# Kernel optimization log

Hardware: AMD Instinct MI355X
Metric: run time of the kernel (lower is better)

The kernel has to match this reference:

```python
import jax, jax.numpy as jnp
import numpy as np


def setup_inputs() -> dict:
    key = jax.random.key(0)
    ks = jax.random.split(key, 5)
    B, S, E, H = 2, 2048, 1024, 16
    scale = 1.0 / np.sqrt(E)
    return {
        "input": jax.random.normal(ks[0], (B, S, E), dtype=jnp.float32),
        "Wqkv": jax.random.normal(ks[1], (3 * E, E), dtype=jnp.float32) * scale,
        "bqkv": jax.random.normal(ks[2], (3 * E,), dtype=jnp.float32) * 0.01,
        "Wo": jax.random.normal(ks[3], (E, E), dtype=jnp.float32) * scale,
        "bo": jax.random.normal(ks[4], (E,), dtype=jnp.float32) * 0.01,
    }


def reference(input, Wqkv, bqkv, Wo, bo):
    H = 16
    B, S, E = input.shape
    dh = E // H
    # fused QKV projection: [B, S, 3E]
    qkv = input @ Wqkv.T + bqkv
    qkv = qkv.reshape(B, S, 3, H, dh)
    qkv = jnp.transpose(qkv, (2, 0, 3, 1, 4))  # [3, B, H, S, dh]
    q, k, v = qkv[0], qkv[1], qkv[2]
    # scores [B, H, Sq, Sk]
    scores = jnp.einsum("bhqd,bhkd->bhqk", q, k) / jnp.sqrt(jnp.float32(dh))
    # NOTE: original code softmaxes over dim=2 (the QUERY axis) — reproduced faithfully
    attn = jax.nn.softmax(scores, axis=2)
    out = jnp.einsum("bhqk,bhkd->bhqd", attn, v)  # [B, H, S, dh]
    out = jnp.transpose(out, (0, 2, 1, 3)).reshape(B, S, E)
    return out @ Wo.T + bo
```

## Files before the change

kernel.cpp:

```cpp
#include <hip/hip_runtime.h>
#include <math.h>

#define B_ 2
#define S_ 2048
#define E_ 1024
#define H_ 16
#define DH_ 64
#define NE3_ 3072
#define MTOT_ (B_*S_)
#define QSCALE_ 0.18033688011112042f

typedef __bf16 bf16;
typedef bf16 bf16x8 __attribute__((ext_vector_type(8)));
typedef bf16 bf16x4 __attribute__((ext_vector_type(4)));
typedef float f32x4 __attribute__((ext_vector_type(4)));

#define MFMA16(a,b,c) __builtin_amdgcn_mfma_f32_16x16x32_bf16(a,b,c,0,0,0)

#define F_(r) ((((r) & 7) ^ (((r) >> 3) & 7)))

__device__ inline void* lds_swz(void* base, int row, int bytecol) {
    return (char*)base + row * 128 + (bytecol ^ (F_(row) << 4));
}

__device__ inline unsigned cvt_pk_bf16(float lo, float hi) {
    unsigned r;
    asm("v_cvt_pk_bf16_f32 %0, %1, %2" : "=v"(r) : "v"(lo), "v"(hi));
    return r;
}

__device__ inline float exp2_hw(float x) {
    float r;
    asm("v_exp_f32 %0, %1" : "=v"(r) : "v"(x));
    return r;
}

__device__ inline void gload_lds16(const void* g, void* l) {
    __builtin_amdgcn_global_load_lds(
        (const __attribute__((address_space(1))) void*)g,
        (__attribute__((address_space(3))) void*)l, 16, 0, 0);
}

#define NX_ (MTOT_*E_)
#define NW_ (NE3_*E_)
#define NWO_ (E_*E_)
__global__ void k_f2b3(const float* __restrict__ x, const float* __restrict__ wq,
                       const float* __restrict__ wo,
                       bf16* __restrict__ xb, bf16* __restrict__ wqb,
                       bf16* __restrict__ wob) {
    const int i = blockIdx.x * 256 + threadIdx.x;
    const int idx = i * 4;
    const float* src; bf16* dst; int off;
    if (idx < NX_)            { src = x;  dst = xb;  off = idx; }
    else if (idx < NX_ + NW_) { src = wq; dst = wqb; off = idx - NX_; }
    else                      { src = wo; dst = wob; off = idx - NX_ - NW_; }
    float4 f = *reinterpret_cast<const float4*>(src + off);
    bf16x4 o;
    o[0] = (bf16)f.x; o[1] = (bf16)f.y; o[2] = (bf16)f.z; o[3] = (bf16)f.w;
    *reinterpret_cast<bf16x4*>(dst + off) = o;
}

template<int MODE>
__global__ __launch_bounds__(256) void k_gemm(
    const bf16* __restrict__ A, const bf16* __restrict__ W,
    const float* __restrict__ bias,
    bf16* __restrict__ Qf, bf16* __restrict__ Kf, bf16* __restrict__ Vf,
    float* __restrict__ out)
{
    constexpr int NBUF = (MODE == 0) ? 1 : 2;
    __shared__ __align__(16) bf16 At[NBUF][128*64];
    __shared__ __align__(16) bf16 Bt[NBUF][128*64];
    const int tid = threadIdx.x, lane = tid & 63, w = tid >> 6;
    const int lq = lane & 15, lh = lane >> 4;
    const int wr = w >> 1, wc = w & 1;
    const int g = blockIdx.x;
    const int nxw = (MODE == 0 ? 3 : 1);
    const int xcd = g & 7, li = g >> 3;
    const int m0 = (li & 31) * 128;
    const int n0 = (xcd * nxw + (li >> 5)) * 128;

    f32x4 acc[4][4] = {};
    const int lrow = lane >> 3, lcol = (lane & 7) * 8;

    auto stage = [&](int k0, int buf) {
        for (int c4 = 0; c4 < 4; ++c4) {
            const int c = w * 4 + c4;
            const int row = c * 8 + lrow;
            const int colx = lcol ^ (F_(row) * 8);
            gload_lds16(A + (size_t)(m0 + row) * E_ + k0 + colx, &At[buf][c * 512]);
            gload_lds16(W + (size_t)(n0 + row) * E_ + k0 + colx, &Bt[buf][c * 512]);
        }
    };
    auto compute = [&](int buf) {
        for (int ks = 0; ks < 2; ++ks) {
            const int bc = ks * 64 + 16 * lh;
            bf16x8 a[4], b[4];
            for (int j = 0; j < 4; ++j)
                a[j] = *(const bf16x8*)lds_swz(&At[buf][0], wr*64 + j*16 + lq, bc);
            for (int i = 0; i < 4; ++i)
                b[i] = *(const bf16x8*)lds_swz(&Bt[buf][0], wc*64 + i*16 + lq, bc);
            for (int i = 0; i < 4; ++i)
                for (int j = 0; j < 4; ++j)
                    acc[i][j] = MFMA16(b[i], a[j], acc[i][j]);
        }
    };

    if constexpr (MODE == 0) {
        stage(0, 0);
        __syncthreads();
        for (int kt = 0; kt < E_/64; ++kt) {
            compute(0);
            if (kt + 1 < E_/64) {
                __syncthreads();
                stage((kt + 1) * 64, 0);
                __syncthreads();
            }
        }
    } else {
        stage(0, 0);
        __syncthreads();
        int cur = 0;
        for (int kt = 0; kt < E_/64; ++kt) {
            if (kt + 1 < E_/64) stage((kt + 1) * 64, cur ^ 1);
            compute(cur);
            cur ^= 1;
            if (kt + 1 < E_/64) __syncthreads();
        }
    }

    const int mW = m0 + wr*64;
    for (int i = 0; i < 4; ++i) {
        const int n4 = n0 + wc*64 + i*16 + lh * 4;
        const float4 b4 = *reinterpret_cast<const float4*>(&bias[n4]);
        const float* bp = reinterpret_cast<const float*>(&b4);
        if constexpr (MODE == 0) {
            const int t = n4 >> 10, h = (n4 >> 6) & 15, d0 = n4 & 63;
            for (int j = 0; j < 4; ++j) {
                const int m = mW + j*16 + lq;
                const int bb_i = m >> 11, s = m & 2047;
                const size_t bh32 = ((size_t)(bb_i*H_ + h)) * 32;
                const int kt = s >> 6;
                if (t == 2) {
                    const int ksV = (s >> 5) & 1, lhV = (s >> 3) & 3, eV = s & 7;
                    for (int r = 0; r < 4; ++r) {
                        const int d = d0 + r;
                        const size_t e = ((bh32 + kt)*8 + (d>>4)*2 + ksV)*512
                                       + (lhV*16 + (d & 15))*8 + eV;
                        Vf[e] = (bf16)(acc[i][j][r] + bp[r]);
                    }
                } else {
                    bf16* dst = (t == 0) ? Qf : Kf;
                    const float sc = (t == 0) ? QSCALE_ : 1.0f;
                    const int kf = (s >> 4) & 3, lqp = s & 15;
                    const size_t e = ((bh32 + kt)*8 + kf*2 + (d0>>5))*512
                                   + (((d0>>3)&3)*16 + lqp)*8 + (d0 & 7);
                    bf16x4 o;
                    for (int r = 0; r < 4; ++r)
                        o[r] = (bf16)((acc[i][j][r] + bp[r]) * sc);
                    *reinterpret_cast<bf16x4*>(dst + e) = o;
                }
            }
        } else {
            for (int j = 0; j < 4; ++j) {
                const int m = mW + j*16 + lq;
                float4 o;
                o.x = acc[i][j][0] + bp[0];
                o.y = acc[i][j][1] + bp[1];
                o.z = acc[i][j][2] + bp[2];
                o.w = acc[i][j][3] + bp[3];
                *reinterpret_cast<float4*>(out + (size_t)m * E_ + n4) = o;
            }
        }
    }
}

__global__ __launch_bounds__(256) void k_colsum(
    const bf16* __restrict__ Qf, const bf16* __restrict__ Kf,
    bf16* __restrict__ Vf)
{
    __shared__ __align__(16) char smem[49152];
    __shared__ float rlbuf[128];
    char* Kl   = smem;
    char* Qbuf = smem + 16384;
    const int tid = threadIdx.x, lane = tid & 63, w = tid >> 6;
    const int l16 = lane * 16;
    const int g = blockIdx.x, xcd = g & 7, li = g >> 3;
    const int bh = xcd * 4 + (li >> 4);
    const int k0 = (li & 15) * 128;
    const bf16* Kbase = Kf + ((size_t)bh*32 + (k0 >> 6)) * 4096;
    const bf16* Qbase = Qf + (size_t)bh*32 * 4096;

    for (int j = 0; j < 4; ++j)
        gload_lds16(Kbase + (j*256 + tid)*8, Kl + (j*256 + w*64)*16);
    auto stageQ = [&](int qt, int buf) {
        const bf16* qb = Qbase + (size_t)qt * 8192;
        for (int j = 0; j < 4; ++j)
            gload_lds16(qb + (j*256 + tid)*8, Qbuf + buf*16384 + (j*256 + w*64)*16);
    };
    stageQ(0, 0);
    __syncthreads();

    bf16x8 bk[2][2];
    for (int f = 0; f < 2; ++f)
        for (int ks = 0; ks < 2; ++ks)
            bk[f][ks] = *(const bf16x8*)(Kl + (w*4 + f*2 + ks)*1024 + l16);

    float lsum0 = 0.f, lsum1 = 0.f;
    int cur = 0;
    for (int qt = 0; qt < S_/128; ++qt) {
        if (qt + 1 < S_/128) stageQ(qt + 1, cur ^ 1);
        #pragma unroll
        for (int qi = 0; qi < 8; ++qi) {
            f32x4 s0 = {}, s1 = {};
            #pragma unroll
            for (int ks = 0; ks < 2; ++ks) {
                bf16x8 aq = *(const bf16x8*)(Qbuf + cur*16384 + (qi*2+ks)*1024 + l16);
                s0 = MFMA16(aq, bk[0][ks], s0);
                s1 = MFMA16(aq, bk[1][ks], s1);
            }
            #pragma unroll
            for (int r = 0; r < 4; ++r) {
                lsum0 += exp2_hw(s0[r]);
                lsum1 += exp2_hw(s1[r]);
            }
        }
        cur ^= 1;
        if (qt + 1 < S_/128) __syncthreads();
    }
    lsum0 += __shfl_xor(lsum0, 16); lsum0 += __shfl_xor(lsum0, 32);
    lsum1 += __shfl_xor(lsum1, 16); lsum1 += __shfl_xor(lsum1, 32);
    if (lane < 16) {
        rlbuf[w*32 + lane]      = 1.0f / lsum0;
        rlbuf[w*32 + 16 + lane] = 1.0f / lsum1;
    }
    __syncthreads();

    bf16* Vb = Vf + ((size_t)bh*32 + (k0 >> 6)) * 4096;
    for (int c = 0; c < 4; ++c) {
        const int v = c*256 + tid;
        const int kb = (v >> 9)*64 + ((v >> 6) & 1)*32 + ((v >> 4) & 3)*8;
        bf16x8* p = reinterpret_cast<bf16x8*>(Vb + v*8);
        bf16x8 x = *p, o;
        #pragma unroll
        for (int jj = 0; jj < 8; ++jj)
            o[jj] = (bf16)((float)x[jj] * rlbuf[kb + jj]);
        *p = o;
    }
}

__global__ __launch_bounds__(256) void k_attn(
    const bf16* __restrict__ Qf, const bf16* __restrict__ Kf,
    const bf16* __restrict__ Vf, bf16* __restrict__ AO)
{
    __shared__ __align__(16) char smem[49152];
    char* QP   = smem;
    char* Kbuf = smem + 16384;
    char* Vbuf = smem + 32768;
    const int tid = threadIdx.x, lane = tid & 63, w = tid >> 6;
    const int lq = lane & 15, lh = lane >> 4;
    const int l16 = lane * 16;
    const int g = blockIdx.x, xcd = g & 7, li = g >> 3;
    const int bh = xcd * 4 + (li >> 4);
    const int q0 = (li & 15) * 128;
    const bf16* Qbase = Qf + ((size_t)bh*32 + (q0 >> 6)) * 4096;
    const bf16* KVof  = (const bf16*)0;
    const bf16* Kbase = Kf + (size_t)bh*32 * 4096;
    const bf16* Vbase = Vf + (size_t)bh*32 * 4096;
    char* Plw = QP + w * 4096;
    const int pOff = (lh >> 1) * 256 + lq * 16 + (lh & 1) * 8;

    for (int j = 0; j < 4; ++j)
        gload_lds16(Qbase + (j*256 + tid)*8, QP + (j*256 + w*64)*16);
    auto stageKV = [&](int kt, int buf) {
        const bf16* kb = Kbase + (size_t)kt * 4096;
        const bf16* vb = Vbase + (size_t)kt * 4096;
        for (int j = 0; j < 2; ++j) {
            gload_lds16(kb + (j*256 + tid)*8, Kbuf + buf*8192 + (j*256 + w*64)*16);
            gload_lds16(vb + (j*256 + tid)*8, Vbuf + buf*8192 + (j*256 + w*64)*16);
        }
    };
    stageKV(0, 0);
    __syncthreads();

    bf16x8 bq[2][2];
    for (int qi = 0; qi < 2; ++qi)
        for (int ks = 0; ks < 2; ++ks)
            bq[qi][ks] = *(const bf16x8*)(QP + w*4096 + (qi*2+ks)*1024 + l16);

    f32x4 oacc[4][2] = {};
    int cur = 0;
    for (int kt = 0; kt < S_/64; ++kt) {
        if (kt + 1 < S_/64) stageKV(kt + 1, cur ^ 1);
        char* Kc = Kbuf + cur*8192;
        char* Vc = Vbuf + cur*8192;

        #pragma unroll
        for (int kf = 0; kf < 4; ++kf) {
            f32x4 sacc[2] = {};
            #pragma unroll
            for (int ks = 0; ks < 2; ++ks) {
                bf16x8 ak = *(const bf16x8*)(Kc + (kf*2+ks)*1024 + l16);
                #pragma unroll
                for (int qi = 0; qi < 2; ++qi)
                    sacc[qi] = MFMA16(ak, bq[qi][ks], sacc[qi]);
            }
            #pragma unroll
            for (int qi = 0; qi < 2; ++qi) {
                uint2 pw;
                pw.x = cvt_pk_bf16(exp2_hw(sacc[qi][0]), exp2_hw(sacc[qi][1]));
                pw.y = cvt_pk_bf16(exp2_hw(sacc[qi][2]), exp2_hw(sacc[qi][3]));
                *(uint2*)(Plw + pOff + (kf>>1)*2048 + (kf&1)*512 + qi*1024) = pw;
            }
        }

        #pragma unroll
        for (int ks = 0; ks < 2; ++ks) {
            bf16x8 av[4], bp[2];
            #pragma unroll
            for (int df = 0; df < 4; ++df)
                av[df] = *(const bf16x8*)(Vc + (df*2+ks)*1024 + l16);
            #pragma unroll
            for (int qi = 0; qi < 2; ++qi)
                bp[qi] = *(const bf16x8*)(Plw + (ks*2+qi)*1024 + l16);
            #pragma unroll
            for (int df = 0; df < 4; ++df)
                #pragma unroll
                for (int qi = 0; qi < 2; ++qi)
                    oacc[df][qi] = MFMA16(av[df], bp[qi], oacc[df][qi]);
        }
        cur ^= 1;
        if (kt + 1 < S_/64) __syncthreads();
    }

    const int b = bh >> 4, h = bh & 15;
    #pragma unroll
    for (int df = 0; df < 4; ++df)
        #pragma unroll
        for (int qi = 0; qi < 2; ++qi) {
            const int d0 = df*16 + lh * 4;
            const int q = q0 + w*32 + qi*16 + lq;
            bf16x4 o;
            for (int r = 0; r < 4; ++r) o[r] = (bf16)oacc[df][qi][r];
            *reinterpret_cast<bf16x4*>(
                AO + ((size_t)(b*S_ + q))*E_ + h*DH_ + d0) = o;
        }
}

extern "C" void kernel_launch(void* const* d_in, const int* in_sizes, int n_in,
                              void* d_out, int out_size, void* d_ws, size_t ws_size,
                              hipStream_t stream) {
    const float* input = (const float*)d_in[0];
    const float* Wqkv  = (const float*)d_in[1];
    const float* bqkv  = (const float*)d_in[2];
    const float* Wo    = (const float*)d_in[3];
    const float* bo    = (const float*)d_in[4];
    float* out = (float*)d_out;

    char* ws = (char*)d_ws;
    bf16*  Xb   = (bf16*) (ws + 0);
    bf16*  Wqb  = (bf16*) (ws + 8388608);
    bf16*  Wob  = (bf16*) (ws + 14680064);
    bf16*  Qfg  = (bf16*) (ws + 16777216);
    bf16*  Kfg  = (bf16*) (ws + 25165824);
    bf16*  Vfg  = (bf16*) (ws + 33554432);
    bf16*  AO   = (bf16*) (ws + 41943040);

    k_f2b3<<<(NX_ + NW_ + NWO_) / 1024, 256, 0, stream>>>(
        input, Wqkv, Wo, Xb, Wqb, Wob);

    k_gemm<0><<<768, 256, 0, stream>>>(Xb, Wqb, bqkv, Qfg, Kfg, Vfg, nullptr);

    k_colsum<<<512, 256, 0, stream>>>(Qfg, Kfg, Vfg);

    k_attn<<<512, 256, 0, stream>>>(Qfg, Kfg, Vfg, AO);

    k_gemm<1><<<256, 256, 0, stream>>>(AO, Wob, bo, nullptr, nullptr, nullptr, out);
}
```

Before: 158.6 us.

## Software-pipeline attention loop: overlap QK/exp of tile t with PV of tile t-1

Restructures the attention main loop so that each iteration computes QK^T and exp for the current K tile while doing the P·V multiply for the previous tile. V gets a triple buffer and P a double buffer per wave. Q is staged through the K buffer and moved into registers up front. The intent is to give the scheduler independent MFMA and transcendental work to interleave, hiding the exp and LDS latency. The cost is more LDS (72KB instead of 48KB), which may lower occupancy, plus extra prologue and epilogue code.

```diff
diff --git a/kernel.cpp b/kernel.cpp
--- a/kernel.cpp
+++ b/kernel.cpp
@@ -252,10 +252,10 @@
     const bf16* __restrict__ Qf, const bf16* __restrict__ Kf,
     const bf16* __restrict__ Vf, bf16* __restrict__ AO)
 {
-    __shared__ __align__(16) char smem[49152];
-    char* QP   = smem;
-    char* Kbuf = smem + 16384;
-    char* Vbuf = smem + 32768;
+    __shared__ __align__(16) char smem[73728];
+    char* Kbuf  = smem;
+    char* Vbuf  = smem + 16384;
+    char* Pbase = smem + 40960;
     const int tid = threadIdx.x, lane = tid & 63, w = tid >> 6;
     const int lq = lane & 15, lh = lane >> 4;
     const int l16 = lane * 16;
@@ -263,37 +263,37 @@
     const int bh = xcd * 4 + (li >> 4);
     const int q0 = (li & 15) * 128;
     const bf16* Qbase = Qf + ((size_t)bh*32 + (q0 >> 6)) * 4096;
-    const bf16* KVof  = (const bf16*)0;
     const bf16* Kbase = Kf + (size_t)bh*32 * 4096;
     const bf16* Vbase = Vf + (size_t)bh*32 * 4096;
-    char* Plw = QP + w * 4096;
     const int pOff = (lh >> 1) * 256 + lq * 16 + (lh & 1) * 8;
 
     for (int j = 0; j < 4; ++j)
-        gload_lds16(Qbase + (j*256 + tid)*8, QP + (j*256 + w*64)*16);
-    auto stageKV = [&](int kt, int buf) {
+        gload_lds16(Qbase + (j*256 + tid)*8, Kbuf + (j*256 + w*64)*16);
+    __syncthreads();
+    bf16x8 bq[2][2];
+    #pragma unroll
+    for (int qi = 0; qi < 2; ++qi)
+        #pragma unroll
+        for (int ks = 0; ks < 2; ++ks)
+            bq[qi][ks] = *(const bf16x8*)(Kbuf + w*4096 + (qi*2+ks)*1024 + l16);
+    __syncthreads();
+
+    auto stageK = [&](int kt, int slot) {
         const bf16* kb = Kbase + (size_t)kt * 4096;
+        for (int j = 0; j < 2; ++j)
+            gload_lds16(kb + (j*256 + tid)*8, Kbuf + slot*8192 + (j*256 + w*64)*16);
+    };
+    auto stageV = [&](int kt, int slot) {
         const bf16* vb = Vbase + (size_t)kt * 4096;
-        for (int j = 0; j < 2; ++j) {
-            gload_lds16(kb + (j*256 + tid)*8, Kbuf + buf*8192 + (j*256 + w*64)*16);
-            gload_lds16(vb + (j*256 + tid)*8, Vbuf + buf*8192 + (j*256 + w*64)*16);
-        }
-    };
-    stageKV(0, 0);
-    __syncthreads();
-
-    bf16x8 bq[2][2];
-    for (int qi = 0; qi < 2; ++qi)
-        for (int ks = 0; ks < 2; ++ks)
-            bq[qi][ks] = *(const bf16x8*)(QP + w*4096 + (qi*2+ks)*1024 + l16);
+        for (int j = 0; j < 2; ++j)
+            gload_lds16(vb + (j*256 + tid)*8, Vbuf + slot*8192 + (j*256 + w*64)*16);
+    };
 
     f32x4 oacc[4][2] = {};
-    int cur = 0;
-    for (int kt = 0; kt < S_/64; ++kt) {
-        if (kt + 1 < S_/64) stageKV(kt + 1, cur ^ 1);
-        char* Kc = Kbuf + cur*8192;
-        char* Vc = Vbuf + cur*8192;
-
+
+    auto QKEXP = [&](int kslot, int ppar) {
+        char* Kc = Kbuf + kslot*8192;
+        char* Pw = Pbase + w*8192 + ppar*4096;
         #pragma unroll
         for (int kf = 0; kf < 4; ++kf) {
             f32x4 sacc[2] = {};
@@ -309,10 +309,13 @@
                 uint2 pw;
                 pw.x = cvt_pk_bf16(exp2_hw(sacc[qi][0]), exp2_hw(sacc[qi][1]));
                 pw.y = cvt_pk_bf16(exp2_hw(sacc[qi][2]), exp2_hw(sacc[qi][3]));
-                *(uint2*)(Plw + pOff + (kf>>1)*2048 + (kf&1)*512 + qi*1024) = pw;
-            }
-        }
-
+                *(uint2*)(Pw + pOff + (kf>>1)*2048 + (kf&1)*512 + qi*1024) = pw;
+            }
+        }
+    };
+    auto PV = [&](int vslot, int ppar) {
+        char* Vc = Vbuf + vslot*8192;
+        char* Pw = Pbase + w*8192 + ppar*4096;
         #pragma unroll
         for (int ks = 0; ks < 2; ++ks) {
             bf16x8 av[4], bp[2];
@@ -321,16 +324,30 @@
                 av[df] = *(const bf16x8*)(Vc + (df*2+ks)*1024 + l16);
             #pragma unroll
             for (int qi = 0; qi < 2; ++qi)
-                bp[qi] = *(const bf16x8*)(Plw + (ks*2+qi)*1024 + l16);
+                bp[qi] = *(const bf16x8*)(Pw + (ks*2+qi)*1024 + l16);
             #pragma unroll
             for (int df = 0; df < 4; ++df)
                 #pragma unroll
                 for (int qi = 0; qi < 2; ++qi)
                     oacc[df][qi] = MFMA16(av[df], bp[qi], oacc[df][qi]);
         }
-        cur ^= 1;
-        if (kt + 1 < S_/64) __syncthreads();
-    }
+    };
+
+    stageK(0, 0); stageV(0, 0);
+    __syncthreads();
+    stageK(1, 1); stageV(1, 1);
+    QKEXP(0, 0);
+    __syncthreads();
+
+    int vprev = 0, vcur = 1, vnext = 2;
+    for (int t = 1; t < 32; ++t) {
+        if (t + 1 < 32) { stageK(t + 1, (t + 1) & 1); stageV(t + 1, vnext); }
+        QKEXP(t & 1, t & 1);
+        PV(vprev, (t - 1) & 1);
+        __syncthreads();
+        const int tmp = vprev; vprev = vcur; vcur = vnext; vnext = tmp;
+    }
+    PV(vprev, 1);
 
     const int b = bh >> 4, h = bh & 15;
     #pragma unroll
```

New measurement: 161.2 us. About the same (+1.6%).

## Switch attention and column-sum kernels to 32x32 MFMA with register-resident P

Applied to the files above, without the earlier changes.

Rewrites the Q/K/V fragment layouts written by the QKV GEMM epilogue to match 32x32x16 MFMA operands. The column-sum and attention kernels now use 32x32 MFMA tiles. In the attention kernel, the exp'd score fragment is repacked in registers via permlane32_swap and fed straight into the PV MFMA instead of going through LDS. It also adds s_setprio around the MFMA bursts. The aim is to remove the LDS round-trip for P and cut per-MFMA issue overhead, at the cost of a riskier layout change across three kernels.

```diff
diff --git a/kernel.cpp b/kernel.cpp
--- a/kernel.cpp
+++ b/kernel.cpp
@@ -14,8 +14,12 @@
 typedef bf16 bf16x8 __attribute__((ext_vector_type(8)));
 typedef bf16 bf16x4 __attribute__((ext_vector_type(4)));
 typedef float f32x4 __attribute__((ext_vector_type(4)));
+typedef float f32x16 __attribute__((ext_vector_type(16)));
+typedef unsigned u32x2 __attribute__((ext_vector_type(2)));
+typedef unsigned u32x4 __attribute__((ext_vector_type(4)));
 
 #define MFMA16(a,b,c) __builtin_amdgcn_mfma_f32_16x16x32_bf16(a,b,c,0,0,0)
+#define MFMA32(a,b,c) __builtin_amdgcn_mfma_f32_32x32x16_bf16(a,b,c,0,0,0)
 
 #define F_(r) ((((r) & 7) ^ (((r) >> 3) & 7)))
 
@@ -27,6 +31,11 @@
     unsigned r;
     asm("v_cvt_pk_bf16_f32 %0, %1, %2" : "=v"(r) : "v"(lo), "v"(hi));
     return r;
+}
+
+__device__ inline void permswap32(unsigned &x, unsigned &y) {
+    u32x2 r = __builtin_amdgcn_permlane32_swap(x, y, false, false);
+    x = r.x; y = r.y;
 }
 
 __device__ inline float exp2_hw(float x) {
@@ -138,22 +147,23 @@
             for (int j = 0; j < 4; ++j) {
                 const int m = mW + j*16 + lq;
                 const int bb_i = m >> 11, s = m & 2047;
-                const size_t bh32 = ((size_t)(bb_i*H_ + h)) * 32;
-                const int kt = s >> 6;
+                const size_t bhb = ((size_t)(bb_i*H_ + h)) * 131072;
                 if (t == 2) {
-                    const int ksV = (s >> 5) & 1, lhV = (s >> 3) & 3, eV = s & 7;
                     for (int r = 0; r < 4; ++r) {
                         const int d = d0 + r;
-                        const size_t e = ((bh32 + kt)*8 + (d>>4)*2 + ksV)*512
-                                       + (lhV*16 + (d & 15))*8 + eV;
+                        const size_t e = bhb + (size_t)(s >> 6) * 4096
+                                       + ((d >> 5) * 4 + ((s >> 4) & 3)) * 512
+                                       + ((d & 31) + 32 * ((s >> 3) & 1)) * 8
+                                       + (s & 7);
                         Vf[e] = (bf16)(acc[i][j][r] + bp[r]);
                     }
                 } else {
                     bf16* dst = (t == 0) ? Qf : Kf;
                     const float sc = (t == 0) ? QSCALE_ : 1.0f;
-                    const int kf = (s >> 4) & 3, lqp = s & 15;
-                    const size_t e = ((bh32 + kt)*8 + kf*2 + (d0>>5))*512
-                                   + (((d0>>3)&3)*16 + lqp)*8 + (d0 & 7);
+                    const size_t e = bhb + (size_t)(s >> 6) * 4096
+                                   + (((s >> 5) & 1) * 4 + (d0 >> 4)) * 512
+                                   + ((s & 31) + 32 * ((d0 >> 3) & 1)) * 8
+                                   + (d0 & 7);
                     bf16x4 o;
                     for (int r = 0; r < 4; ++r)
                         o[r] = (bf16)((acc[i][j][r] + bp[r]) * sc);
@@ -187,8 +197,8 @@
     const int g = blockIdx.x, xcd = g & 7, li = g >> 3;
     const int bh = xcd * 4 + (li >> 4);
     const int k0 = (li & 15) * 128;
-    const bf16* Kbase = Kf + ((size_t)bh*32 + (k0 >> 6)) * 4096;
-    const bf16* Qbase = Qf + (size_t)bh*32 * 4096;
+    const bf16* Kbase = Kf + (size_t)bh * 131072 + (size_t)(k0 >> 6) * 4096;
+    const bf16* Qbase = Qf + (size_t)bh * 131072;
 
     for (int j = 0; j < 4; ++j)
         gload_lds16(Kbase + (j*256 + tid)*8, Kl + (j*256 + w*64)*16);
@@ -200,45 +210,41 @@
     stageQ(0, 0);
     __syncthreads();
 
-    bf16x8 bk[2][2];
-    for (int f = 0; f < 2; ++f)
-        for (int ks = 0; ks < 2; ++ks)
-            bk[f][ks] = *(const bf16x8*)(Kl + (w*4 + f*2 + ks)*1024 + l16);
-
-    float lsum0 = 0.f, lsum1 = 0.f;
+    bf16x8 bk[4];
+    #pragma unroll
+    for (int sl = 0; sl < 4; ++sl)
+        bk[sl] = *(const bf16x8*)(Kl + w*4096 + sl*1024 + l16);
+
+    float lsum = 0.f;
     int cur = 0;
     for (int qt = 0; qt < S_/128; ++qt) {
         if (qt + 1 < S_/128) stageQ(qt + 1, cur ^ 1);
         #pragma unroll
-        for (int qi = 0; qi < 8; ++qi) {
-            f32x4 s0 = {}, s1 = {};
-            #pragma unroll
-            for (int ks = 0; ks < 2; ++ks) {
-                bf16x8 aq = *(const bf16x8*)(Qbuf + cur*16384 + (qi*2+ks)*1024 + l16);
-                s0 = MFMA16(aq, bk[0][ks], s0);
-                s1 = MFMA16(aq, bk[1][ks], s1);
-            }
-            #pragma unroll
-            for (int r = 0; r < 4; ++r) {
-                lsum0 += exp2_hw(s0[r]);
-                lsum1 += exp2_hw(s1[r]);
-            }
+        for (int qs = 0; qs < 4; ++qs) {
+            f32x16 s = {};
+            __builtin_amdgcn_s_setprio(1);
+            #pragma unroll
+            for (int sl = 0; sl < 4; ++sl) {
+                bf16x8 aq = *(const bf16x8*)(Qbuf + cur*16384 + (qs*4+sl)*1024 + l16);
+                s = MFMA32(aq, bk[sl], s);
+            }
+            __builtin_amdgcn_s_setprio(0);
+            #pragma unroll
+            for (int r = 0; r < 16; ++r)
+                lsum += exp2_hw(s[r]);
         }
         cur ^= 1;
         if (qt + 1 < S_/128) __syncthreads();
     }
-    lsum0 += __shfl_xor(lsum0, 16); lsum0 += __shfl_xor(lsum0, 32);
-    lsum1 += __shfl_xor(lsum1, 16); lsum1 += __shfl_xor(lsum1, 32);
-    if (lane < 16) {
-        rlbuf[w*32 + lane]      = 1.0f / lsum0;
-        rlbuf[w*32 + 16 + lane] = 1.0f / lsum1;
-    }
+    lsum += __shfl_xor(lsum, 32);
+    if (lane < 32)
+        rlbuf[w*32 + lane] = 1.0f / lsum;
     __syncthreads();
 
-    bf16* Vb = Vf + ((size_t)bh*32 + (k0 >> 6)) * 4096;
+    bf16* Vb = Vf + (size_t)bh * 131072 + (size_t)(k0 >> 6) * 4096;
     for (int c = 0; c < 4; ++c) {
         const int v = c*256 + tid;
-        const int kb = (v >> 9)*64 + ((v >> 6) & 1)*32 + ((v >> 4) & 3)*8;
+        const int kb = (v >> 9)*64 + ((v >> 6) & 3)*16 + ((v >> 5) & 1)*8;
         bf16x8* p = reinterpret_cast<bf16x8*>(Vb + v*8);
         bf16x8 x = *p, o;
         #pragma unroll
@@ -257,17 +263,13 @@
     char* Kbuf = smem + 16384;
     char* Vbuf = smem + 32768;
     const int tid = threadIdx.x, lane = tid & 63, w = tid >> 6;
-    const int lq = lane & 15, lh = lane >> 4;
     const int l16 = lane * 16;
     const int g = blockIdx.x, xcd = g & 7, li = g >> 3;
     const int bh = xcd * 4 + (li >> 4);
     const int q0 = (li & 15) * 128;
-    const bf16* Qbase = Qf + ((size_t)bh*32 + (q0 >> 6)) * 4096;
-    const bf16* KVof  = (const bf16*)0;
-    const bf16* Kbase = Kf + (size_t)bh*32 * 4096;
-    const bf16* Vbase = Vf + (size_t)bh*32 * 4096;
-    char* Plw = QP + w * 4096;
-    const int pOff = (lh >> 1) * 256 + lq * 16 + (lh & 1) * 8;
+    const bf16* Qbase = Qf + (size_t)bh * 131072 + (size_t)(q0 >> 6) * 4096;
+    const bf16* Kbase = Kf + (size_t)bh * 131072;
+    const bf16* Vbase = Vf + (size_t)bh * 131072;
 
     for (int j = 0; j < 4; ++j)
         gload_lds16(Qbase + (j*256 + tid)*8, QP + (j*256 + w*64)*16);
@@ -282,67 +284,69 @@
     stageKV(0, 0);
     __syncthreads();
 
-    bf16x8 bq[2][2];
-    for (int qi = 0; qi < 2; ++qi)
-        for (int ks = 0; ks < 2; ++ks)
-            bq[qi][ks] = *(const bf16x8*)(QP + w*4096 + (qi*2+ks)*1024 + l16);
-
-    f32x4 oacc[4][2] = {};
+    bf16x8 bq[4];
+    #pragma unroll
+    for (int sl = 0; sl < 4; ++sl)
+        bq[sl] = *(const bf16x8*)(QP + w*4096 + sl*1024 + l16);
+
+    f32x16 oacc[2] = {};
     int cur = 0;
-    for (int kt = 0; kt < S_/64; ++kt) {
-        if (kt + 1 < S_/64) stageKV(kt + 1, cur ^ 1);
+    for (int t = 0; t < S_/64; ++t) {
+        if (t + 1 < S_/64) stageKV(t + 1, cur ^ 1);
         char* Kc = Kbuf + cur*8192;
         char* Vc = Vbuf + cur*8192;
 
         #pragma unroll
-        for (int kf = 0; kf < 4; ++kf) {
-            f32x4 sacc[2] = {};
-            #pragma unroll
-            for (int ks = 0; ks < 2; ++ks) {
-                bf16x8 ak = *(const bf16x8*)(Kc + (kf*2+ks)*1024 + l16);
+        for (int kt = 0; kt < 2; ++kt) {
+            f32x16 s = {};
+            __builtin_amdgcn_s_setprio(1);
+            #pragma unroll
+            for (int sl = 0; sl < 4; ++sl) {
+                bf16x8 ak = *(const bf16x8*)(Kc + (kt*4+sl)*1024 + l16);
+                s = MFMA32(ak, bq[sl], s);
+            }
+            __builtin_amdgcn_s_setprio(0);
+
+            unsigned a[8];
+            #pragma unroll
+            for (int gg = 0; gg < 8; ++gg)
+                a[gg] = cvt_pk_bf16(exp2_hw(s[2*gg]), exp2_hw(s[2*gg+1]));
+
+            #pragma unroll
+            for (int kl = 0; kl < 2; ++kl) {
+                unsigned m0 = a[4*kl + 0], m2 = a[4*kl + 2];
+                unsigned m1 = a[4*kl + 1], m3 = a[4*kl + 3];
+                permswap32(m0, m2);
+                permswap32(m1, m3);
+                u32x4 pw = {m0, m1, m2, m3};
+                bf16x8 pf = __builtin_bit_cast(bf16x8, pw);
+                const int ksl = kt*2 + kl;
+                __builtin_amdgcn_s_setprio(1);
                 #pragma unroll
-                for (int qi = 0; qi < 2; ++qi)
-                    sacc[qi] = MFMA16(ak, bq[qi][ks], sacc[qi]);
-            }
-            #pragma unroll
-            for (int qi = 0; qi < 2; ++qi) {
-                uint2 pw;
-                pw.x = cvt_pk_bf16(exp2_hw(sacc[qi][0]), exp2_hw(sacc[qi][1]));
-                pw.y = cvt_pk_bf16(exp2_hw(sacc[qi][2]), exp2_hw(sacc[qi][3]));
-                *(uint2*)(Plw + pOff + (kf>>1)*2048 + (kf&1)*512 + qi*1024) = pw;
-            }
-        }
-
+                for (int dt = 0; dt < 2; ++dt) {
+                    bf16x8 av = *(const bf16x8*)(Vc + (dt*4+ksl)*1024 + l16);
+                    oacc[dt] = MFMA32(av, pf, oacc[dt]);
+                }
+                __builtin_amdgcn_s_setprio(0);
+            }
+        }
+        cur ^= 1;
+        if (t + 1 < S_/64) __syncthreads();
+    }
+
+    const int b = bh >> 4, h = bh & 15;
+    const int q = q0 + w*32 + (lane & 31);
+    const int hi4 = (lane >> 5) * 4;
+    bf16* aob = AO + ((size_t)(b*S_ + q))*E_ + h*DH_;
+    #pragma unroll
+    for (int dt = 0; dt < 2; ++dt)
         #pragma unroll
-        for (int ks = 0; ks < 2; ++ks) {
-            bf16x8 av[4], bp[2];
-            #pragma unroll
-            for (int df = 0; df < 4; ++df)
-                av[df] = *(const bf16x8*)(Vc + (df*2+ks)*1024 + l16);
-            #pragma unroll
-            for (int qi = 0; qi < 2; ++qi)
-                bp[qi] = *(const bf16x8*)(Plw + (ks*2+qi)*1024 + l16);
-            #pragma unroll
-            for (int df = 0; df < 4; ++df)
-                #pragma unroll
-                for (int qi = 0; qi < 2; ++qi)
-                    oacc[df][qi] = MFMA16(av[df], bp[qi], oacc[df][qi]);
-        }
-        cur ^= 1;
-        if (kt + 1 < S_/64) __syncthreads();
-    }
-
-    const int b = bh >> 4, h = bh & 15;
-    #pragma unroll
-    for (int df = 0; df < 4; ++df)
-        #pragma unroll
-        for (int qi = 0; qi < 2; ++qi) {
-            const int d0 = df*16 + lh * 4;
-            const int q = q0 + w*32 + qi*16 + lq;
+        for (int rg = 0; rg < 4; ++rg) {
+            const int dbase = dt*32 + 8*rg + hi4;
             bf16x4 o;
-            for (int r = 0; r < 4; ++r) o[r] = (bf16)oacc[df][qi][r];
-            *reinterpret_cast<bf16x4*>(
-                AO + ((size_t)(b*S_ + q))*E_ + h*DH_ + d0) = o;
+            #pragma unroll
+            for (int r = 0; r < 4; ++r) o[r] = (bf16)oacc[dt][rg*4 + r];
+            *reinterpret_cast<bf16x4*>(aob + dbase) = o;
         }
 }
 
```

Result: faster. 153.6 us (-3.1%).
